# Kernel optimization log

Measured on AMD Instinct MI355X. Metric: run time of the kernel, lower is better.

## Reference

```python
import jax, jax.numpy as jnp
import numpy as np

B, T, E = 2, 2048, 2048
H = 16
DH = E // H  # 128
FFN = 4 * E  # 8192
EPS = 1e-5


def _layernorm(x, g, b):
    mu = jnp.mean(x, axis=-1, keepdims=True)
    var = jnp.mean((x - mu) ** 2, axis=-1, keepdims=True)
    return (x - mu) * jax.lax.rsqrt(var + EPS) * g + b


def setup_inputs() -> dict:
    key = jax.random.key(0)
    ks = jax.random.split(key, 8)
    s = 0.02
    return {
        "x": jax.random.normal(ks[0], (B, T, E), jnp.float32),
        "g1": jnp.ones((E,), jnp.float32),
        "b1": jnp.zeros((E,), jnp.float32),
        "wq": jax.random.normal(ks[1], (E, E), jnp.float32) * s,
        "wk": jax.random.normal(ks[2], (E, E), jnp.float32) * s,
        "wv": jax.random.normal(ks[3], (E, E), jnp.float32) * s,
        "wo": jax.random.normal(ks[4], (E, E), jnp.float32) * s,
        "g2": jnp.ones((E,), jnp.float32),
        "b2": jnp.zeros((E,), jnp.float32),
        "w1": jax.random.normal(ks[5], (E, FFN), jnp.float32) * s,
        "w2": jax.random.normal(ks[6], (E, FFN), jnp.float32) * s,
        "w3": jax.random.normal(ks[7], (FFN, E), jnp.float32) * s,
    }


def reference(x, g1, b1, wq, wk, wv, wo, g2, b2, w1, w2, w3):
    Bx, Tx, Ex = x.shape
    # --- attention block (pre-LN, residual) ---
    h = _layernorm(x, g1, b1)
    q = (h @ wq).reshape(Bx, Tx, H, DH)
    k = (h @ wk).reshape(Bx, Tx, H, DH)
    v = (h @ wv).reshape(Bx, Tx, H, DH)
    scores = jnp.einsum('bqhd,bkhd->bhqk', q, k) / jnp.sqrt(jnp.float32(DH))
    causal = jnp.tril(jnp.ones((Tx, Tx), bool))  # [T,T]
    scores = jnp.where(causal[None, None], scores, -jnp.inf)
    attn = jax.nn.softmax(scores, axis=-1)
    ctx = jnp.einsum('bhqk,bkhd->bqhd', attn, v).reshape(Bx, Tx, H * DH)
    x = x + ctx @ wo
    # --- SwiGLU MLP block (pre-LN, residual) ---
    h = _layernorm(x, g2, b2)
    gated = jax.nn.silu(h @ w1) * (h @ w2)
    return x + gated @ w3
```

## Files before the change

### kernel.cpp

```cpp
#include <hip/hip_runtime.h>


#define T_SEQ 2048
#define E_DIM 2048
#define N_HEAD 16
#define D_HEAD 128
#define FFN_DIM 8192
#define M_ROWS 4096
#define QS (3 * E_DIM)

typedef unsigned short u16;
typedef short short8 __attribute__((ext_vector_type(8)));
typedef float f32x4 __attribute__((ext_vector_type(4)));

#define DEV __device__ __forceinline__

DEV u16 f2bf(float f) {
  unsigned u = __float_as_uint(f);
  u += 0x7fffu + ((u >> 16) & 1u);
  return (u16)(u >> 16);
}
DEV float bf2f(u16 h) { return __uint_as_float(((unsigned)h) << 16); }

DEV void async16(void* lds, const void* g) {
  __builtin_amdgcn_global_load_lds((const __attribute__((address_space(1))) void*)g,
                                   (__attribute__((address_space(3))) void*)lds, 16, 0, 0);
}

__global__ __launch_bounds__(256) void ln_kernel(const float* __restrict__ x,
                                                 const float* __restrict__ gw,
                                                 const float* __restrict__ bw,
                                                 u16* __restrict__ out) {
  int row = blockIdx.x;
  int t = threadIdx.x;
  const float4* xr = (const float4*)(x + (size_t)row * E_DIM);
  float4 a = xr[t], c = xr[t + 256];
  float s = a.x + a.y + a.z + a.w + c.x + c.y + c.z + c.w;
  float q = a.x * a.x + a.y * a.y + a.z * a.z + a.w * a.w +
            c.x * c.x + c.y * c.y + c.z * c.z + c.w * c.w;
  for (int off = 32; off > 0; off >>= 1) {
    s += __shfl_down(s, off);
    q += __shfl_down(q, off);
  }
  __shared__ float red[8];
  if ((t & 63) == 0) { red[(t >> 6) * 2] = s; red[(t >> 6) * 2 + 1] = q; }
  __syncthreads();
  s = red[0] + red[2] + red[4] + red[6];
  q = red[1] + red[3] + red[5] + red[7];
  float mu = s * (1.f / E_DIM);
  float rs = rsqrtf(q * (1.f / E_DIM) - mu * mu + 1e-5f);
  const float4* g4 = (const float4*)gw;
  const float4* b4 = (const float4*)bw;
  float4 g0 = g4[t], g1v = g4[t + 256], e0 = b4[t], e1 = b4[t + 256];
  ushort4 o0, o1;
  o0.x = f2bf((a.x - mu) * rs * g0.x + e0.x);
  o0.y = f2bf((a.y - mu) * rs * g0.y + e0.y);
  o0.z = f2bf((a.z - mu) * rs * g0.z + e0.z);
  o0.w = f2bf((a.w - mu) * rs * g0.w + e0.w);
  o1.x = f2bf((c.x - mu) * rs * g1v.x + e1.x);
  o1.y = f2bf((c.y - mu) * rs * g1v.y + e1.y);
  o1.z = f2bf((c.z - mu) * rs * g1v.z + e1.z);
  o1.w = f2bf((c.w - mu) * rs * g1v.w + e1.w);
  ((ushort4*)(out + (size_t)row * E_DIM))[t] = o0;
  ((ushort4*)(out + (size_t)row * E_DIM))[t + 256] = o1;
}

__global__ __launch_bounds__(256) void cvt_t_kernel(const float* __restrict__ W,
                                                    u16* __restrict__ WT,
                                                    int Kd, int Nd) {
  __shared__ float tile[32][33];
  int tx = threadIdx.x, ty = threadIdx.y;
  int n0 = blockIdx.x * 32, k0 = blockIdx.y * 32;
#pragma unroll
  for (int i = 0; i < 4; i++)
    tile[ty + i * 8][tx] = W[(size_t)(k0 + ty + i * 8) * Nd + n0 + tx];
  __syncthreads();
#pragma unroll
  for (int i = 0; i < 4; i++)
    WT[(size_t)(n0 + ty + i * 8) * Kd + k0 + tx] = f2bf(tile[tx][ty + i * 8]);
}

__global__ __launch_bounds__(256) void transpose_v_kernel(const u16* __restrict__ qkv,
                                                          u16* __restrict__ vt) {
  __shared__ u16 tile[32][33];
  int tx = threadIdx.x, ty = threadIdx.y;
  int b = blockIdx.z;
  int t0 = blockIdx.x * 32, e0 = blockIdx.y * 32;
#pragma unroll
  for (int i = 0; i < 4; i++)
    tile[ty + i * 8][tx] =
        qkv[(size_t)(b * T_SEQ + t0 + ty + i * 8) * QS + 2 * E_DIM + e0 + tx];
  __syncthreads();
#pragma unroll
  for (int i = 0; i < 4; i++)
    vt[((size_t)b * E_DIM + e0 + ty + i * 8) * T_SEQ + t0 + tx] = tile[tx][ty + i * 8];
}

template <int MODE, int BM_>
__global__ __launch_bounds__(512, 1) void gemm8p(const u16* __restrict__ A,
                                                 const u16* __restrict__ BT,
                                                 void* __restrict__ Cout,
                                                 const void* __restrict__ Extra,
                                                 int N, int K, int colMajorXcd) {
  constexpr int MM = BM_ / 64;
  constexpr int AUNIT = BM_ * 32;
  __shared__ u16 Abuf[4 * AUNIT];
  __shared__ u16 Bbuf[4 * 8192];
  const int t = threadIdx.x;
  const int w = t >> 6, l = t & 63, g = l >> 4, lq = l & 15;
  const int wm = w >> 2, wn = w & 3;

  const int gx = gridDim.x, gy = gridDim.y;
  const int nwg = gx * gy;
  int lin = colMajorXcd ? (blockIdx.x * gy + blockIdx.y)
                        : (blockIdx.y * gx + blockIdx.x);
  const int qq = nwg >> 3;
  int wg = (lin & 7) * qq + (lin >> 3);
  int bx, by;
  if (colMajorXcd) { bx = wg / gy; by = wg - bx * gy; }
  else             { by = wg / gx; bx = wg - by * gx; }
  const size_t bm = (size_t)by * BM_, bn = (size_t)bx * 256;

  const int srcrow = ((l >> 3) << 1) | (l & 1);
  const int csrc = ((((l >> 1) & 3) ^ ((l >> 3) & 3)) << 3);
  const u16* aSrc = A + (bm + w * 16 + srcrow) * (size_t)K + csrc;
  const u16* bSrc = BT + (bn + w * 16 + srcrow) * (size_t)K + csrc;
  const int rdoff = (((lq & 1) + 2 * (g ^ ((lq >> 1) & 3))) << 3);

#define STA8(DB, KS, TILE)                                                    \
  {                                                                           \
    u16* Ad = Abuf + (DB) * (2 * AUNIT) + (KS)*AUNIT + w * 512;               \
    const u16* as_ = aSrc + (size_t)(TILE)*64 + (KS)*32;                      \
    async16(Ad, as_);                                                         \
    if constexpr (BM_ == 256) async16(Ad + 4096, as_ + (size_t)128 * K);      \
  }
#define STB8(DB, KS, TILE)                                                    \
  {                                                                           \
    u16* Bd = Bbuf + (DB)*16384 + (KS)*8192 + w * 512;                        \
    const u16* bs_ = bSrc + (size_t)(TILE)*64 + (KS)*32;                      \
    async16(Bd, bs_);                                                         \
    async16(Bd + 4096, bs_ + (size_t)128 * K);                                \
  }
#define RDA8(DB, KS, MH)                                                      \
  _Pragma("unroll") for (int mm = 0; mm < MM; ++mm)                           \
      af[mm] = *(const short8*)(Abuf + (DB) * (2 * AUNIT) + (KS)*AUNIT +      \
                                (wm * (BM_ / 4) + (MH) * (BM_ / 8) + mm * 8 + \
                                 (lq >> 1)) * 64 + rdoff);
#define RDB8(DB, KS)                                                          \
  _Pragma("unroll") for (int nn = 0; nn < 4; ++nn)                            \
      bf[nn] = *(const short8*)(Bbuf + (DB)*16384 + (KS)*8192 +               \
                                (wn * 32 + nn * 8 + (lq >> 1)) * 64 + rdoff);
#define MM168(MH)                                                             \
  _Pragma("unroll") for (int mm = 0; mm < MM; ++mm)                           \
      _Pragma("unroll") for (int nn = 0; nn < 4; ++nn)                        \
          acc[(MH)*MM + mm][nn] = __builtin_amdgcn_mfma_f32_16x16x32_bf16(    \
              af[mm], bf[nn], acc[(MH)*MM + mm][nn], 0, 0, 0);
#define SYNCA                                                                 \
  asm volatile("s_barrier" ::: "memory");                                     \
  asm volatile("s_waitcnt lgkmcnt(0)" ::: "memory");                          \
  __builtin_amdgcn_sched_barrier(0);                                          \
  __builtin_amdgcn_s_setprio(1);
#define ENDP __builtin_amdgcn_s_setprio(0);
#define BAR2 asm volatile("s_barrier" ::: "memory");
#define WAITN                                                                 \
  if constexpr (BM_ == 256) asm volatile("s_waitcnt vmcnt(8)" ::: "memory");  \
  else                      asm volatile("s_waitcnt vmcnt(6)" ::: "memory");
#define WAITH                                                                 \
  if constexpr (BM_ == 256) asm volatile("s_waitcnt vmcnt(4)" ::: "memory");  \
  else                      asm volatile("s_waitcnt vmcnt(3)" ::: "memory");

  const int NT = K >> 6, NI = NT >> 1;
  f32x4 acc[2 * MM][4] = {};
  short8 af[MM > 4 ? MM : 4], bf[4];

  STA8(0, 0, 0); STB8(0, 0, 0);
  STA8(0, 1, 0); STB8(0, 1, 0);
  STA8(1, 0, 1); STB8(1, 0, 1);
  WAITN;
  BAR2;

  for (int j = 0; j < NI; ++j) {
    const int t1 = 2 * j + 1, t2 = 2 * j + 2, t3 = 2 * j + 3;
    const bool s2 = t2 < NT, s3 = t3 < NT, lastI = (j + 1 == NI);
    RDB8(0, 0); RDA8(0, 0, 0);
    STA8(1, 1, t1);
    SYNCA; MM168(0); ENDP; BAR2;
    RDA8(0, 0, 1);
    STB8(1, 1, t1);
    SYNCA; MM168(1); ENDP;
    WAITN;
    BAR2;
    RDB8(0, 1); RDA8(0, 1, 0);
    if (s2) STA8(0, 0, t2);
    SYNCA; MM168(0); ENDP; BAR2;
    RDA8(0, 1, 1);
    if (s2) STB8(0, 0, t2);
    SYNCA; MM168(1); ENDP;
    if (lastI) { WAITH; } else { WAITN; }
    BAR2;
    RDB8(1, 0); RDA8(1, 0, 0);
    if (s2) STA8(0, 1, t2);
    SYNCA; MM168(0); ENDP; BAR2;
    RDA8(1, 0, 1);
    if (s2) STB8(0, 1, t2);
    SYNCA; MM168(1); ENDP;
    if (lastI) { asm volatile("s_waitcnt vmcnt(0)" ::: "memory"); } else { WAITN; }
    BAR2;
    RDB8(1, 1); RDA8(1, 1, 0);
    if (s3) STA8(1, 0, t3);
    SYNCA; MM168(0); ENDP; BAR2;
    RDA8(1, 1, 1);
    if (s3) STB8(1, 0, t3);
    SYNCA; MM168(1); ENDP;
    if (!lastI) { WAITN; }
    BAR2;
  }
#undef STA8
#undef STB8
#undef RDA8
#undef RDB8
#undef MM168
#undef SYNCA
#undef ENDP
#undef BAR2
#undef WAITN
#undef WAITH

#pragma unroll
  for (int m = 0; m < 2 * MM; m++) {
    size_t row = bm + wm * (BM_ / 2) + m * 16 + 4 * g;
#pragma unroll
    for (int n = 0; n < 4; n++) {
      size_t col = bn + wn * 64 + n * 16 + lq;
#pragma unroll
      for (int r = 0; r < 4; r++) {
        size_t idx = (row + r) * (size_t)N + col;
        if constexpr (MODE == 0) {
          ((u16*)Cout)[idx] = f2bf(acc[m][n][r]);
        } else if constexpr (MODE == 1) {
          ((float*)Cout)[idx] = ((const float*)Extra)[idx] + acc[m][n][r];
        } else {
          float a = bf2f(((const u16*)Extra)[idx]);
          float sil = a / (1.f + exp2f(-1.4426950408889634f * a));
          ((u16*)Cout)[idx] = f2bf(sil * acc[m][n][r]);
        }
      }
    }
  }
}

__global__ __launch_bounds__(256, 3) void attn_kernel(const u16* __restrict__ QKV,
                                                      const u16* __restrict__ VT,
                                                      u16* __restrict__ CTX) {
  __shared__ u16 Ks[64 * 128];
  __shared__ u16 Vs[128 * 64];
  __shared__ u16 P_all[4][16 * 72];
  const int t = threadIdx.x;
  const int w = t >> 6, l = t & 63, g = l >> 4, lq = l & 15;
  u16* P = P_all[w];
  const int q0blk = blockIdx.x * 64;
  const int q0w = q0blk + w * 16;
  const int bh = blockIdx.y, b = bh >> 4, h = bh & 15;
  const u16* qp = QKV + (size_t)b * T_SEQ * QS + h * D_HEAD;
  const u16* kp = QKV + (size_t)b * T_SEQ * QS + E_DIM + h * D_HEAD;
  const u16* vp = VT + ((size_t)b * E_DIM + h * D_HEAD) * T_SEQ;

  short8 qf[4];
#pragma unroll
  for (int ks = 0; ks < 4; ks++)
    qf[ks] = *(const short8*)(qp + (size_t)(q0w + lq) * QS + ks * 32 + g * 8);

  f32x4 acc[8] = {};
  float m2[4], ls[4];
#pragma unroll
  for (int r = 0; r < 4; r++) { m2[r] = -1e30f; ls[r] = 0.f; }
  const float sc = 0.08838834764831845f * 1.4426950408889634f;

  const int kRow0 = 16 * w + (l >> 4);
  const int kChunk = l & 15;
  const int vRow0 = 32 * w + (l >> 3);
  const int vChunk = l & 7;

  for (int kv0 = 0; kv0 <= q0blk; kv0 += 64) {
#pragma unroll
    for (int j = 0; j < 4; j++) {
      int R = kRow0 + 4 * j;
      async16(Ks + (16 * w + 4 * j) * 128,
              kp + (size_t)(kv0 + R) * QS + ((kChunk ^ (R & 7)) << 3));
    }
#pragma unroll
    for (int j = 0; j < 4; j++) {
      int D = vRow0 + 8 * j;
      async16(Vs + (32 * w + 8 * j) * 64,
              vp + (size_t)D * T_SEQ + kv0 + ((vChunk ^ (D & 7)) << 3));
    }
    __syncthreads();

    f32x4 s[4];
#pragma unroll
    for (int ct = 0; ct < 4; ct++) {
      s[ct] = f32x4{0.f, 0.f, 0.f, 0.f};
#pragma unroll
      for (int ks = 0; ks < 4; ks++) {
        short8 kf = *(const short8*)(Ks + (ct * 16 + lq) * 128 +
                                     (((ks * 4 + g) ^ (lq & 7)) << 3));
        s[ct] = __builtin_amdgcn_mfma_f32_16x16x32_bf16(qf[ks], kf, s[ct], 0, 0, 0);
      }
    }
    float sv[4][4];
#pragma unroll
    for (int ct = 0; ct < 4; ct++)
#pragma unroll
      for (int r = 0; r < 4; r++) sv[ct][r] = s[ct][r] * sc;
    if (kv0 + 64 > q0w) {
#pragma unroll
      for (int ct = 0; ct < 4; ct++)
#pragma unroll
        for (int r = 0; r < 4; r++)
          if (kv0 + ct * 16 + lq > q0w + 4 * g + r) sv[ct][r] = -1e30f;
    }
    float mx[4];
#pragma unroll
    for (int r = 0; r < 4; r++)
      mx[r] = fmaxf(fmaxf(sv[0][r], sv[1][r]), fmaxf(sv[2][r], sv[3][r]));
#pragma unroll
    for (int off = 1; off < 16; off <<= 1)
#pragma unroll
      for (int r = 0; r < 4; r++) mx[r] = fmaxf(mx[r], __shfl_xor(mx[r], off));
#pragma unroll
    for (int r = 0; r < 4; r++) {
      float mn = fmaxf(m2[r], mx[r]);
      float sca = exp2f(m2[r] - mn);
      m2[r] = mn;
      float sum = 0.f;
#pragma unroll
      for (int ct = 0; ct < 4; ct++) {
        float pv = exp2f(sv[ct][r] - mn);
        sum += pv;
        P[(4 * g + r) * 72 + ct * 16 + lq] = f2bf(pv);
      }
      ls[r] = ls[r] * sca + sum;
#pragma unroll
      for (int n = 0; n < 8; n++) acc[n][r] *= sca;
    }
    short8 pa[2];
#pragma unroll
    for (int ks2 = 0; ks2 < 2; ks2++)
      pa[ks2] = *(const short8*)(P + lq * 72 + ks2 * 32 + g * 8);
#pragma unroll
    for (int n = 0; n < 8; n++)
#pragma unroll
      for (int ks2 = 0; ks2 < 2; ks2++) {
        short8 vf = *(const short8*)(Vs + (n * 16 + lq) * 64 +
                                     (((ks2 * 4 + g) ^ (lq & 7)) << 3));
        acc[n] = __builtin_amdgcn_mfma_f32_16x16x32_bf16(pa[ks2], vf, acc[n], 0, 0, 0);
      }
    __syncthreads();
  }

#pragma unroll
  for (int off = 1; off < 16; off <<= 1)
#pragma unroll
    for (int r = 0; r < 4; r++) ls[r] += __shfl_xor(ls[r], off);
  float inv[4];
#pragma unroll
  for (int r = 0; r < 4; r++) inv[r] = 1.f / ls[r];
  u16* cp = CTX + ((size_t)b * T_SEQ + q0w) * E_DIM + h * D_HEAD;
#pragma unroll
  for (int n = 0; n < 8; n++)
#pragma unroll
    for (int r = 0; r < 4; r++)
      cp[(size_t)(4 * g + r) * E_DIM + n * 16 + lq] = f2bf(acc[n][r] * inv[r]);
}

extern "C" void kernel_launch(void* const* d_in, const int* in_sizes, int n_in,
                              void* d_out, int out_size, void* d_ws, size_t ws_size,
                              hipStream_t stream) {
  (void)in_sizes; (void)n_in; (void)out_size; (void)ws_size;
  const float* x  = (const float*)d_in[0];
  const float* g1 = (const float*)d_in[1];
  const float* b1 = (const float*)d_in[2];
  const float* wq = (const float*)d_in[3];
  const float* wk = (const float*)d_in[4];
  const float* wv = (const float*)d_in[5];
  const float* wo = (const float*)d_in[6];
  const float* g2 = (const float*)d_in[7];
  const float* b2 = (const float*)d_in[8];
  const float* w1 = (const float*)d_in[9];
  const float* w2 = (const float*)d_in[10];
  const float* w3 = (const float*)d_in[11];
  float* out = (float*)d_out;

  const size_t EE2 = (size_t)E_DIM * E_DIM * 2;
  const size_t EF2 = (size_t)E_DIM * FFN_DIM * 2;
  const size_t ME2 = (size_t)M_ROWS * E_DIM * 2;
  char* p = (char*)d_ws;
  u16* wqkvT = (u16*)p; p += 3 * EE2;
  u16* woT = (u16*)p; p += EE2;
  u16* w1T = (u16*)p; p += EF2;
  u16* w2T = (u16*)p; p += EF2;
  u16* w3T = (u16*)p; p += EF2;
  u16* Hb  = (u16*)p; p += ME2;
  u16* QKVb = (u16*)p; p += (size_t)M_ROWS * QS * 2;
  u16* VTb = (u16*)p; p += ME2;
  u16* CTXb = (u16*)p; p += ME2;
  u16* U1b = QKVb;

  dim3 blk32(32, 8);
  cvt_t_kernel<<<dim3(E_DIM / 32, E_DIM / 32), blk32, 0, stream>>>(wq, wqkvT, E_DIM, E_DIM);
  cvt_t_kernel<<<dim3(E_DIM / 32, E_DIM / 32), blk32, 0, stream>>>(wk, wqkvT + E_DIM * E_DIM, E_DIM, E_DIM);
  cvt_t_kernel<<<dim3(E_DIM / 32, E_DIM / 32), blk32, 0, stream>>>(wv, wqkvT + 2 * E_DIM * E_DIM, E_DIM, E_DIM);
  cvt_t_kernel<<<dim3(E_DIM / 32, E_DIM / 32), blk32, 0, stream>>>(wo, woT, E_DIM, E_DIM);
  cvt_t_kernel<<<dim3(FFN_DIM / 32, E_DIM / 32), blk32, 0, stream>>>(w1, w1T, E_DIM, FFN_DIM);
  cvt_t_kernel<<<dim3(FFN_DIM / 32, E_DIM / 32), blk32, 0, stream>>>(w2, w2T, E_DIM, FFN_DIM);
  cvt_t_kernel<<<dim3(E_DIM / 32, FFN_DIM / 32), blk32, 0, stream>>>(w3, w3T, FFN_DIM, E_DIM);

  ln_kernel<<<M_ROWS, 256, 0, stream>>>(x, g1, b1, Hb);
  gemm8p<0, 128><<<dim3(QS / 256, M_ROWS / 128), 512, 0, stream>>>(Hb, wqkvT, QKVb, nullptr, QS, E_DIM, 1);
  transpose_v_kernel<<<dim3(T_SEQ / 32, E_DIM / 32, 2), blk32, 0, stream>>>(QKVb, VTb);
  attn_kernel<<<dim3(T_SEQ / 64, 2 * N_HEAD), 256, 0, stream>>>(QKVb, VTb, CTXb);
  gemm8p<1, 128><<<dim3(E_DIM / 256, M_ROWS / 128), 512, 0, stream>>>(CTXb, woT, out, x, E_DIM, E_DIM, 1);

  ln_kernel<<<M_ROWS, 256, 0, stream>>>(out, g2, b2, Hb);
  gemm8p<0, 256><<<dim3(FFN_DIM / 256, M_ROWS / 256), 512, 0, stream>>>(Hb, w1T, U1b, nullptr, FFN_DIM, E_DIM, 1);
  gemm8p<2, 256><<<dim3(FFN_DIM / 256, M_ROWS / 256), 512, 0, stream>>>(Hb, w2T, U1b, U1b, FFN_DIM, E_DIM, 1);
  gemm8p<1, 128><<<dim3(E_DIM / 256, M_ROWS / 128), 512, 0, stream>>>(U1b, w3T, out, out, E_DIM, FFN_DIM, 1);
}
```

Baseline: 960.3 us.

## Add four-phase pipelined GEMM kernel for QKV, output and down projections

Introduces a specialized 128x256 GEMM kernel that splits each K tile into two substeps and overlaps async global-to-LDS loads with register fragment reads and MFMA work across four phases per iteration, using explicit vmcnt waits, barriers and wave priority hints. It replaces the generic gemm8p for the QKV projection, attention output projection and MLP down projection. The aim is to hide memory latency better and cut barrier stalls. The cost is a more intricate hand-scheduled kernel whose waitcnt counts must stay exactly matched to the number of issued loads.

```diff
diff --git a/kernel.cpp b/kernel.cpp
--- a/kernel.cpp
+++ b/kernel.cpp
@@ -94,6 +94,131 @@
 #pragma unroll
   for (int i = 0; i < 4; i++)
     vt[((size_t)b * E_DIM + e0 + ty + i * 8) * T_SEQ + t0 + tx] = tile[tx][ty + i * 8];
+}
+
+template <int MODE>
+__global__ __launch_bounds__(512, 1) void gemm4p(const u16* __restrict__ A,
+                                                 const u16* __restrict__ BT,
+                                                 void* __restrict__ Cout,
+                                                 const void* __restrict__ Extra,
+                                                 int N, int K, int colMajorXcd) {
+  __shared__ u16 Abuf[4 * 4096];
+  __shared__ u16 Bbuf[4 * 8192];
+  const int t = threadIdx.x;
+  const int w = t >> 6, l = t & 63, g = l >> 4, lq = l & 15;
+  const int wm = w >> 2, wn = w & 3;
+
+  const int gx = gridDim.x, gy = gridDim.y;
+  const int nwg = gx * gy;
+  int lin = colMajorXcd ? (blockIdx.x * gy + blockIdx.y)
+                        : (blockIdx.y * gx + blockIdx.x);
+  const int qq = nwg >> 3;
+  int wg = (lin & 7) * qq + (lin >> 3);
+  int bx, by;
+  if (colMajorXcd) { bx = wg / gy; by = wg - bx * gy; }
+  else             { by = wg / gx; bx = wg - by * gx; }
+  const size_t bm = (size_t)by * 128, bn = (size_t)bx * 256;
+
+  const int srcrow = ((l >> 3) << 1) | (l & 1);
+  const int csrc = ((((l >> 1) & 3) ^ ((l >> 3) & 3)) << 3);
+  const u16* aSrc = A + (bm + w * 16 + srcrow) * (size_t)K + csrc;
+  const u16* bSrc = BT + (bn + w * 16 + srcrow) * (size_t)K + csrc;
+  const int rdoff = (((lq & 1) + 2 * (g ^ ((lq >> 1) & 3))) << 3);
+
+#define STA(DB, KS, TILE)                                                     \
+  async16(Abuf + (DB)*8192 + (KS)*4096 + w * 512,                             \
+          aSrc + (size_t)(TILE)*64 + (KS)*32);
+#define STB(DB, KS, TILE)                                                     \
+  {                                                                           \
+    u16* Bd = Bbuf + (DB)*16384 + (KS)*8192 + w * 512;                        \
+    const u16* bs_ = bSrc + (size_t)(TILE)*64 + (KS)*32;                      \
+    async16(Bd, bs_);                                                         \
+    async16(Bd + 4096, bs_ + (size_t)128 * K);                                \
+  }
+#define RD_A(DST, DB, KS)                                                     \
+  _Pragma("unroll") for (int m2 = 0; m2 < 4; ++m2)                            \
+      DST[m2] = *(const short8*)(Abuf + (DB)*8192 + (KS)*4096 +               \
+                                 (wm * 32 + m2 * 8 + (lq >> 1)) * 64 + rdoff);
+#define RD_B(DST, DB, KS)                                                     \
+  _Pragma("unroll") for (int nn = 0; nn < 4; ++nn)                            \
+      DST[nn] = *(const short8*)(Bbuf + (DB)*16384 + (KS)*8192 +              \
+                                 (wn * 32 + nn * 8 + (lq >> 1)) * 64 + rdoff);
+#define MMA(AF, BF)                                                           \
+  _Pragma("unroll") for (int m2 = 0; m2 < 4; ++m2)                            \
+      _Pragma("unroll") for (int nn = 0; nn < 4; ++nn)                        \
+          acc[m2][nn] = __builtin_amdgcn_mfma_f32_16x16x32_bf16(              \
+              AF[m2], BF[nn], acc[m2][nn], 0, 0, 0);
+#define ENDPH(VN_STR)                                                         \
+  __builtin_amdgcn_s_setprio(0);                                              \
+  __builtin_amdgcn_sched_barrier(0);                                          \
+  asm volatile("s_waitcnt vmcnt(" VN_STR ")" ::: "memory");                   \
+  asm volatile("s_barrier" ::: "memory");
+
+  const int NT = K >> 6, NI = NT >> 1;
+  f32x4 acc[4][4] = {};
+  short8 af0[4], bf0[4], af1[4], bf1[4];
+
+  STA(0, 0, 0); STB(0, 0, 0);
+  STA(0, 1, 0); STB(0, 1, 0);
+  STA(1, 0, 1); STB(1, 0, 1);
+  asm volatile("s_waitcnt vmcnt(3)" ::: "memory");
+  asm volatile("s_barrier" ::: "memory");
+  RD_A(af0, 0, 0); RD_B(bf0, 0, 0);
+
+  for (int j = 0; j < NI; ++j) {
+    const int tb = 2 * j + 1, t2 = 2 * j + 2, t3 = 2 * j + 3;
+    const bool li = (j + 1 == NI);
+    RD_A(af1, 0, 1); RD_B(bf1, 0, 1);
+    STA(1, 1, tb); STB(1, 1, tb);
+    __builtin_amdgcn_s_setprio(1);
+    MMA(af0, bf0);
+    ENDPH("3")
+    RD_A(af0, 1, 0); RD_B(bf0, 1, 0);
+    if (!li) { STA(0, 0, t2); STB(0, 0, t2); }
+    __builtin_amdgcn_s_setprio(1);
+    MMA(af1, bf1);
+    if (!li) { ENDPH("3") } else { ENDPH("0") }
+    RD_A(af1, 1, 1); RD_B(bf1, 1, 1);
+    if (!li) { STA(0, 1, t2); STB(0, 1, t2); }
+    __builtin_amdgcn_s_setprio(1);
+    MMA(af0, bf0);
+    if (!li) { ENDPH("3") } else { ENDPH("0") }
+    if (!li) {
+      RD_A(af0, 0, 0); RD_B(bf0, 0, 0);
+      STA(1, 0, t3); STB(1, 0, t3);
+    }
+    __builtin_amdgcn_s_setprio(1);
+    MMA(af1, bf1);
+    if (!li) { ENDPH("3") } else { __builtin_amdgcn_s_setprio(0); }
+  }
+#undef STA
+#undef STB
+#undef RD_A
+#undef RD_B
+#undef MMA
+#undef ENDPH
+
+#pragma unroll
+  for (int m = 0; m < 4; m++) {
+    size_t row = bm + wm * 64 + m * 16 + 4 * g;
+#pragma unroll
+    for (int n = 0; n < 4; n++) {
+      size_t col = bn + wn * 64 + n * 16 + lq;
+#pragma unroll
+      for (int r = 0; r < 4; r++) {
+        size_t idx = (row + r) * (size_t)N + col;
+        if constexpr (MODE == 0) {
+          ((u16*)Cout)[idx] = f2bf(acc[m][n][r]);
+        } else if constexpr (MODE == 1) {
+          ((float*)Cout)[idx] = ((const float*)Extra)[idx] + acc[m][n][r];
+        } else {
+          float a = bf2f(((const u16*)Extra)[idx]);
+          float sil = a / (1.f + exp2f(-1.4426950408889634f * a));
+          ((u16*)Cout)[idx] = f2bf(sil * acc[m][n][r]);
+        }
+      }
+    }
+  }
 }
 
 template <int MODE, int BM_>
@@ -416,13 +541,13 @@
   cvt_t_kernel<<<dim3(E_DIM / 32, FFN_DIM / 32), blk32, 0, stream>>>(w3, w3T, FFN_DIM, E_DIM);
 
   ln_kernel<<<M_ROWS, 256, 0, stream>>>(x, g1, b1, Hb);
-  gemm8p<0, 128><<<dim3(QS / 256, M_ROWS / 128), 512, 0, stream>>>(Hb, wqkvT, QKVb, nullptr, QS, E_DIM, 1);
+  gemm4p<0><<<dim3(QS / 256, M_ROWS / 128), 512, 0, stream>>>(Hb, wqkvT, QKVb, nullptr, QS, E_DIM, 1);
   transpose_v_kernel<<<dim3(T_SEQ / 32, E_DIM / 32, 2), blk32, 0, stream>>>(QKVb, VTb);
   attn_kernel<<<dim3(T_SEQ / 64, 2 * N_HEAD), 256, 0, stream>>>(QKVb, VTb, CTXb);
-  gemm8p<1, 128><<<dim3(E_DIM / 256, M_ROWS / 128), 512, 0, stream>>>(CTXb, woT, out, x, E_DIM, E_DIM, 1);
+  gemm4p<1><<<dim3(E_DIM / 256, M_ROWS / 128), 512, 0, stream>>>(CTXb, woT, out, x, E_DIM, E_DIM, 1);
 
   ln_kernel<<<M_ROWS, 256, 0, stream>>>(out, g2, b2, Hb);
   gemm8p<0, 256><<<dim3(FFN_DIM / 256, M_ROWS / 256), 512, 0, stream>>>(Hb, w1T, U1b, nullptr, FFN_DIM, E_DIM, 1);
   gemm8p<2, 256><<<dim3(FFN_DIM / 256, M_ROWS / 256), 512, 0, stream>>>(Hb, w2T, U1b, U1b, FFN_DIM, E_DIM, 1);
-  gemm8p<1, 128><<<dim3(E_DIM / 256, M_ROWS / 128), 512, 0, stream>>>(U1b, w3T, out, out, E_DIM, FFN_DIM, 1);
-}
+  gemm4p<1><<<dim3(E_DIM / 256, M_ROWS / 128), 512, 0, stream>>>(U1b, w3T, out, out, E_DIM, FFN_DIM, 1);
+}
```

After: 973.7 us. About the same (+1.4%).
